# Kernel optimization log

Hardware: AMD Instinct MI355X
Metric: run time of the kernel (lower is better)

Reference implementation:

```python
import jax, jax.numpy as jnp
import numpy as np

ND, NW, E, D, DOUT = 20000, 30000, 500000, 256, 256


def setup_inputs() -> dict:
    key = jax.random.key(0)
    ks = jax.random.split(key, 10)
    inp = {
        "doc_hidden": jax.random.normal(ks[0], (ND, D), dtype=jnp.float32),
        "word_hidden": jax.random.normal(ks[1], (NW, D), dtype=jnp.float32),
        "edge_doc": jax.random.randint(ks[2], (E,), 0, ND),
        "edge_word": jax.random.randint(ks[3], (E,), 0, NW),
        # attn_fc_d2w / attn_fc_w2d: Linear(2*D, 1)
        "attn_d2w_w": jax.random.normal(ks[4], (2 * D, 1), dtype=jnp.float32) / np.sqrt(2 * D),
        "attn_d2w_b": jnp.zeros((1,), dtype=jnp.float32),
        "attn_w2d_w": jax.random.normal(ks[5], (2 * D, 1), dtype=jnp.float32) / np.sqrt(2 * D),
        "attn_w2d_b": jnp.zeros((1,), dtype=jnp.float32),
        # fc: Linear(D, DOUT), shared by doc and word outputs
        "fc_w": jax.random.normal(ks[6], (D, DOUT), dtype=jnp.float32) / np.sqrt(D),
        "fc_b": jnp.zeros((DOUT,), dtype=jnp.float32),
    }
    return inp


def _segment_softmax(e, seg, n):
    # e: [E] edge scores, seg: [E] destination ids -> per-dst softmax
    m = jax.ops.segment_max(e, seg, num_segments=n)
    ex = jnp.exp(e - m[seg])
    s = jax.ops.segment_sum(ex, seg, num_segments=n)
    return ex / jnp.maximum(s[seg], 1e-30)


def _gat_direction(z_src_nodes, z_dst_nodes, src_idx, dst_idx, w, b, n_dst):
    D_ = z_src_nodes.shape[1]
    zs = z_src_nodes[src_idx]                      # [E, D]
    zd = z_dst_nodes[dst_idx]                      # [E, D]
    # concat([zs, zd]) @ w == zs @ w[:D] + zd @ w[D:]
    a = zs @ w[:D_] + zd @ w[D_:] + b              # [E, 1]
    e = jax.nn.leaky_relu(a[:, 0], negative_slope=0.01)  # [E]
    alpha = _segment_softmax(e, dst_idx, n_dst)    # [E]
    return jax.ops.segment_sum(alpha[:, None] * zs, dst_idx, num_segments=n_dst)


def reference(doc_hidden, word_hidden, edge_doc, edge_word,
              attn_d2w_w, attn_d2w_b, attn_w2d_w, attn_w2d_b, fc_w, fc_b):
    # 'include': doc -> word aggregation into word nodes
    word_h = _gat_direction(doc_hidden, word_hidden, edge_doc, edge_word,
                            attn_d2w_w, attn_d2w_b, NW)
    # 'included': word -> doc aggregation into doc nodes
    doc_h = _gat_direction(word_hidden, doc_hidden, edge_word, edge_doc,
                           attn_w2d_w, attn_w2d_b, ND)
    # shared fc; dropout is identity in eval; softmax over feature dim (dim=1)
    doc_out = jax.nn.softmax(doc_h @ fc_w + fc_b, axis=1)
    word_out = jax.nn.softmax(word_h @ fc_w + fc_b, axis=1)
    return doc_out, word_out
```

## Files before the change

### kernel.cpp

```cpp
#include <hip/hip_runtime.h>

constexpr int ND_N = 20000;
constexpr int NW_N = 30000;
constexpr int NE_E = 500000;
constexpr int DDIM = 256;
constexpr int MROWS = ND_N + NW_N;

constexpr int SB = 64;

constexpr float QSCALE = 32767.f / 8.f;
constexpr float DQSCALE = 8.f / 32767.f;

constexpr int LROW = DDIM + 8;

constexpr int EDGE_BLOCKS = (NE_E + 255) / 256;
constexpr int NODE_BLOCKS = (MROWS + 3) / 4;
constexpr int CONV_BLOCKS = DDIM;

typedef __attribute__((ext_vector_type(8))) short short8v;
typedef __attribute__((ext_vector_type(4))) float f32x4;
typedef __attribute__((ext_vector_type(4))) short s16x4;
typedef __attribute__((ext_vector_type(4))) unsigned short us4;

__device__ __forceinline__ float lrelu(float x) { return x > 0.f ? x : 0.01f * x; }
__device__ __forceinline__ unsigned short f2bf(float x) {
  unsigned u = __float_as_uint(x);
  return (unsigned short)((u + 0x7FFFu + ((u >> 16) & 1u)) >> 16);
}
__device__ __forceinline__ float bf2f(unsigned short h) {
  return __uint_as_float(((unsigned)h) << 16);
}
__device__ __forceinline__ short q16(float x) {
  float c = fminf(fmaxf(x, -8.f), 8.f);
  return (short)__float2int_rn(c * QSCALE);
}

__global__ __launch_bounds__(256) void prep_all(
    const float* __restrict__ doc, const float* __restrict__ word,
    const float* __restrict__ d2w_w, const float* __restrict__ w2d_w,
    const float* __restrict__ fc_w,
    const int* __restrict__ ed, const int* __restrict__ ew,
    float* __restrict__ s1, float* __restrict__ t2,
    float* __restrict__ s2, float* __restrict__ t1,
    short* __restrict__ doc_q, short* __restrict__ word_q,
    int* __restrict__ pos1, int* __restrict__ pos2,
    unsigned short* __restrict__ bkt1, unsigned short* __restrict__ bkt2,
    unsigned short* __restrict__ whi, unsigned short* __restrict__ wlo) {
  int b = blockIdx.x;
  if (b < EDGE_BLOCKS) {
    int i = b * 256 + threadIdx.x;
    if (i >= NE_E) return;
    int d = ed[i], w = ew[i];
    int p1 = atomicAdd(&pos1[w], 1);
    p1 = min(p1, SB - 1);
    __builtin_nontemporal_store((unsigned short)d, &bkt1[(size_t)w * SB + p1]);
    int p2 = atomicAdd(&pos2[d], 1);
    p2 = min(p2, SB - 1);
    __builtin_nontemporal_store((unsigned short)w, &bkt2[(size_t)d * SB + p2]);
  } else if (b < EDGE_BLOCKS + NODE_BLOCKS) {
    int wid = (b - EDGE_BLOCKS) * 4 + (threadIdx.x >> 6);
    int lane = threadIdx.x & 63;
    if (wid >= MROWS) return;
    const float* h;
    const float* wa;
    const float* wb;
    float* oa;
    float* ob;
    short* qdst;
    int idx;
    if (wid < ND_N) {
      idx = wid;
      h = doc + (size_t)idx * DDIM;
      wa = d2w_w;
      wb = w2d_w + DDIM;
      oa = s1;
      ob = t2;
      qdst = doc_q;
    } else {
      idx = wid - ND_N;
      h = word + (size_t)idx * DDIM;
      wa = w2d_w;
      wb = d2w_w + DDIM;
      oa = s2;
      ob = t1;
      qdst = word_q;
    }
    const float4 z = *(const float4*)&h[lane * 4];
    const float4 a4 = *(const float4*)&wa[lane * 4];
    const float4 b4 = *(const float4*)&wb[lane * 4];
    s16x4 zq;
    zq.x = q16(z.x);
    zq.y = q16(z.y);
    zq.z = q16(z.z);
    zq.w = q16(z.w);
    *(s16x4*)&qdst[(size_t)idx * DDIM + lane * 4] = zq;
    float pa = z.x * a4.x + z.y * a4.y + z.z * a4.z + z.w * a4.w;
    float pb = z.x * b4.x + z.y * b4.y + z.z * b4.z + z.w * b4.w;
#pragma unroll
    for (int o = 32; o > 0; o >>= 1) {
      pa += __shfl_xor(pa, o);
      pb += __shfl_xor(pb, o);
    }
    if (lane == 0) {
      oa[idx] = pa;
      ob[idx] = pb;
    }
  } else {
    int k = b - EDGE_BLOCKS - NODE_BLOCKS;
    int n = threadIdx.x;
    float x = fc_w[(size_t)k * DDIM + n];
    unsigned short h = f2bf(x);
    float lo = x - bf2f(h);
    whi[(size_t)n * DDIM + k] = h;
    wlo[(size_t)n * DDIM + k] = f2bf(lo);
  }
}

__global__ __launch_bounds__(256) void aggregate_all(
    const short* __restrict__ doc_q, const short* __restrict__ word_q,
    const unsigned short* __restrict__ bkt1, const unsigned short* __restrict__ bkt2,
    const int* __restrict__ pos1, const int* __restrict__ pos2,
    const float* __restrict__ s1, const float* __restrict__ t1,
    const float* __restrict__ s2, const float* __restrict__ t2,
    const float* __restrict__ b1p, const float* __restrict__ b2p,
    float* __restrict__ out) {
  int wid = (blockIdx.x * blockDim.x + threadIdx.x) >> 6;
  int lane = threadIdx.x & 63;
  if (wid >= MROWS) return;
  const short* src;
  const unsigned short* bkt;
  const float* sS;
  float tval, bval;
  int cnt, row;
  if (wid < NW_N) {
    src = doc_q;
    bkt = bkt1 + (size_t)wid * SB;
    cnt = min(pos1[wid], SB);
    sS = s1;
    tval = t1[wid];
    bval = b1p[0];
    row = ND_N + wid;
  } else {
    int d = wid - NW_N;
    src = word_q;
    bkt = bkt2 + (size_t)d * SB;
    cnt = min(pos2[d], SB);
    sS = s2;
    tval = t2[d];
    bval = b2p[0];
    row = d;
  }
  int sidx = 0;
  float v = 0.f;
  if (lane < cnt) {
    sidx = bkt[lane];
    v = __expf(lrelu(sS[sidx] + tval + bval));
  }
  float vsum = v;
  float ax = 0.f, ay = 0.f, az = 0.f, aw = 0.f;
  int t = 0;
  for (; t + 16 <= cnt; t += 16) {
    s16x4 z16[16];
    float vv[16];
#pragma unroll
    for (int q = 0; q < 16; ++q) {
      int ss = __shfl(sidx, t + q);
      vv[q] = __shfl(v, t + q);
      z16[q] = *(const s16x4*)&src[(size_t)ss * DDIM + lane * 4];
    }
#pragma unroll
    for (int q = 0; q < 16; ++q) {
      ax += vv[q] * (float)z16[q].x;
      ay += vv[q] * (float)z16[q].y;
      az += vv[q] * (float)z16[q].z;
      aw += vv[q] * (float)z16[q].w;
    }
  }
  for (; t + 8 <= cnt; t += 8) {
    s16x4 z8[8];
    float vv[8];
#pragma unroll
    for (int q = 0; q < 8; ++q) {
      int ss = __shfl(sidx, t + q);
      vv[q] = __shfl(v, t + q);
      z8[q] = *(const s16x4*)&src[(size_t)ss * DDIM + lane * 4];
    }
#pragma unroll
    for (int q = 0; q < 8; ++q) {
      ax += vv[q] * (float)z8[q].x;
      ay += vv[q] * (float)z8[q].y;
      az += vv[q] * (float)z8[q].z;
      aw += vv[q] * (float)z8[q].w;
    }
  }
  for (; t < cnt; ++t) {
    int ss = __shfl(sidx, t);
    float vv = __shfl(v, t);
    const s16x4 z = *(const s16x4*)&src[(size_t)ss * DDIM + lane * 4];
    ax += vv * (float)z.x;
    ay += vv * (float)z.y;
    az += vv * (float)z.z;
    aw += vv * (float)z.w;
  }
#pragma unroll
  for (int o = 32; o > 0; o >>= 1) vsum += __shfl_xor(vsum, o);
  float inv = DQSCALE / fmaxf(vsum, 1e-30f);
  float4 o4 = {ax * inv, ay * inv, az * inv, aw * inv};
  *(float4*)&out[(size_t)row * DDIM + lane * 4] = o4;
}

__global__ __launch_bounds__(256) void fc_mfma_sm(
    float* __restrict__ y,
    const unsigned short* __restrict__ w_hi_t, const unsigned short* __restrict__ w_lo_t,
    const float* __restrict__ bias, int nrows) {
  __shared__ unsigned short a_hi[32 * LROW];
  __shared__ unsigned short a_lo[32 * LROW];
  __shared__ float lds_max[4][32];
  __shared__ float lds_sum[4][32];
  int tid = threadIdx.x;
  int row0 = blockIdx.x * 32;

  int wv = tid >> 6;
  int l = tid & 63;
  int lr = l & 15;
  int g = l >> 4;
  int lk = g * 8;

  const unsigned short* bh = w_hi_t + (size_t)(wv * 64 + lr) * DDIM + lk;
  const unsigned short* bl = w_lo_t + (size_t)(wv * 64 + lr) * DDIM + lk;
  short8v bHi[2][4], bLo[2][4];
#pragma unroll
  for (int cf = 0; cf < 4; ++cf) {
    bHi[0][cf] = *(const short8v*)(bh + cf * 16 * DDIM);
    bLo[0][cf] = *(const short8v*)(bl + cf * 16 * DDIM);
  }

  {
    int r = tid >> 3;
    int c0 = (tid & 7) * 32;
    int arow = min(row0 + r, nrows - 1);
    const float* srcp = &y[(size_t)arow * DDIM + c0];
    unsigned short* dh = &a_hi[r * LROW + c0];
    unsigned short* dl = &a_lo[r * LROW + c0];
#pragma unroll
    for (int j = 0; j < 8; ++j) {
      float4 f = *(const float4*)&srcp[j * 4];
      float fv[4] = {f.x, f.y, f.z, f.w};
      us4 h4, l4;
#pragma unroll
      for (int c = 0; c < 4; ++c) {
        unsigned short hb = f2bf(fv[c]);
        h4[c] = hb;
        l4[c] = f2bf(fv[c] - bf2f(hb));
      }
      *(us4*)&dh[j * 4] = h4;
      *(us4*)&dl[j * 4] = l4;
    }
  }
  __syncthreads();

  f32x4 acc[2][4];
#pragma unroll
  for (int rf = 0; rf < 2; ++rf)
#pragma unroll
    for (int cf = 0; cf < 4; ++cf) acc[rf][cf] = (f32x4){0.f, 0.f, 0.f, 0.f};

#pragma unroll
  for (int ks = 0; ks < 8; ++ks) {
    const int cur = ks & 1;
    const int nxt = cur ^ 1;
    if (ks < 7) {
#pragma unroll
      for (int cf = 0; cf < 4; ++cf) {
        bHi[nxt][cf] = *(const short8v*)(bh + cf * 16 * DDIM + (ks + 1) * 32);
        bLo[nxt][cf] = *(const short8v*)(bl + cf * 16 * DDIM + (ks + 1) * 32);
      }
    }
    int kbase = ks * 32 + lk;
    short8v aHi[2], aLo[2];
#pragma unroll
    for (int rf = 0; rf < 2; ++rf) {
      int r = rf * 16 + lr;
      aHi[rf] = *(const short8v*)&a_hi[r * LROW + kbase];
      aLo[rf] = *(const short8v*)&a_lo[r * LROW + kbase];
    }
#pragma unroll
    for (int rf = 0; rf < 2; ++rf)
#pragma unroll
      for (int cf = 0; cf < 4; ++cf) {
        acc[rf][cf] = __builtin_amdgcn_mfma_f32_16x16x32_bf16(aHi[rf], bHi[cur][cf], acc[rf][cf], 0, 0, 0);
        acc[rf][cf] = __builtin_amdgcn_mfma_f32_16x16x32_bf16(aLo[rf], bHi[cur][cf], acc[rf][cf], 0, 0, 0);
        acc[rf][cf] = __builtin_amdgcn_mfma_f32_16x16x32_bf16(aHi[rf], bLo[cur][cf], acc[rf][cf], 0, 0, 0);
      }
  }

#pragma unroll
  for (int rf = 0; rf < 2; ++rf)
#pragma unroll
    for (int cf = 0; cf < 4; ++cf) {
      float bc = bias[wv * 64 + cf * 16 + lr];
#pragma unroll
      for (int r = 0; r < 4; ++r) acc[rf][cf][r] += bc;
    }

#pragma unroll
  for (int rf = 0; rf < 2; ++rf)
#pragma unroll
    for (int r = 0; r < 4; ++r) {
      float m = fmaxf(fmaxf(acc[rf][0][r], acc[rf][1][r]), fmaxf(acc[rf][2][r], acc[rf][3][r]));
#pragma unroll
      for (int o = 1; o < 16; o <<= 1) m = fmaxf(m, __shfl_xor(m, o));
      if (lr == 0) lds_max[wv][rf * 16 + g * 4 + r] = m;
    }
  __syncthreads();
#pragma unroll
  for (int rf = 0; rf < 2; ++rf)
#pragma unroll
    for (int r = 0; r < 4; ++r) {
      int idx = rf * 16 + g * 4 + r;
      float m = fmaxf(fmaxf(lds_max[0][idx], lds_max[1][idx]),
                      fmaxf(lds_max[2][idx], lds_max[3][idx]));
      float s = 0.f;
#pragma unroll
      for (int cf = 0; cf < 4; ++cf) {
        float e = __expf(acc[rf][cf][r] - m);
        acc[rf][cf][r] = e;
        s += e;
      }
#pragma unroll
      for (int o = 1; o < 16; o <<= 1) s += __shfl_xor(s, o);
      if (lr == 0) lds_sum[wv][idx] = s;
    }
  __syncthreads();
#pragma unroll
  for (int rf = 0; rf < 2; ++rf)
#pragma unroll
    for (int r = 0; r < 4; ++r) {
      int idx = rf * 16 + g * 4 + r;
      float s = lds_sum[0][idx] + lds_sum[1][idx] + lds_sum[2][idx] + lds_sum[3][idx];
      float inv = 1.f / s;
      int row = row0 + rf * 16 + g * 4 + r;
      if (row < nrows) {
#pragma unroll
        for (int cf = 0; cf < 4; ++cf)
          y[(size_t)row * DDIM + wv * 64 + cf * 16 + lr] = acc[rf][cf][r] * inv;
      }
    }
}

extern "C" void kernel_launch(void* const* d_in, const int* in_sizes, int n_in,
                              void* d_out, int out_size, void* d_ws, size_t ws_size,
                              hipStream_t stream) {
  const float* doc_hidden = (const float*)d_in[0];
  const float* word_hidden = (const float*)d_in[1];
  const int* edge_doc = (const int*)d_in[2];
  const int* edge_word = (const int*)d_in[3];
  const float* d2w_w = (const float*)d_in[4];
  const float* d2w_b = (const float*)d_in[5];
  const float* w2d_w = (const float*)d_in[6];
  const float* w2d_b = (const float*)d_in[7];
  const float* fc_w = (const float*)d_in[8];
  const float* fc_b = (const float*)d_in[9];
  float* out = (float*)d_out;

  char* p = (char*)d_ws;
  auto carveB = [&](size_t bytes) {
    char* r = p;
    p += ((bytes + 255) & ~(size_t)255);
    return r;
  };
  auto carve = [&](size_t elems) { return carveB(elems * 4); };
  float* s1 = (float*)carve(ND_N);
  float* t2 = (float*)carve(ND_N);
  float* s2 = (float*)carve(NW_N);
  float* t1 = (float*)carve(NW_N);
  char* zbeg = p;
  int* pos1 = (int*)carve(NW_N);
  int* pos2 = (int*)carve(ND_N);
  char* zend = p;
  unsigned short* bkt1 = (unsigned short*)carveB((size_t)NW_N * SB * 2);
  unsigned short* bkt2 = (unsigned short*)carveB((size_t)ND_N * SB * 2);
  short* doc_q = (short*)carveB((size_t)ND_N * DDIM * 2);
  short* word_q = (short*)carveB((size_t)NW_N * DDIM * 2);
  unsigned short* w_hi_t = (unsigned short*)carveB((size_t)DDIM * DDIM * 2);
  unsigned short* w_lo_t = (unsigned short*)carveB((size_t)DDIM * DDIM * 2);

  hipMemsetAsync(zbeg, 0, (size_t)(zend - zbeg), stream);

  prep_all<<<EDGE_BLOCKS + NODE_BLOCKS + CONV_BLOCKS, 256, 0, stream>>>(
      doc_hidden, word_hidden, d2w_w, w2d_w, fc_w, edge_doc, edge_word,
      s1, t2, s2, t1, doc_q, word_q, pos1, pos2, bkt1, bkt2, w_hi_t, w_lo_t);

  aggregate_all<<<(MROWS + 3) / 4, 256, 0, stream>>>(doc_q, word_q, bkt1, bkt2, pos1, pos2,
                                                     s1, t1, s2, t2, d2w_b, w2d_b, out);

  fc_mfma_sm<<<(MROWS + 31) / 32, 256, 0, stream>>>(out, w_hi_t, w_lo_t, fc_b, MROWS);
}
```

Measured before the change: 313.9 us.

## Make FC kernel persistent with prefetched double-buffered tiles; pad atomic counters

The FC+softmax kernel now runs as a persistent grid of 521 blocks, each handling 3 row tiles. The next tile's fp32 rows are prefetched into registers during the current tile's MFMA work, then split to bf16 hi/lo into a second LDS buffer. This hides global load latency and cuts block launch overhead. Separately, the per-node edge counters are spaced 16 ints apart (one per 64-byte line) so atomics from different nodes no longer share a cache line. The cost is a 16x larger counter memset and scattered counter reads.

```diff
diff --git a/kernel.cpp b/kernel.cpp
--- a/kernel.cpp
+++ b/kernel.cpp
@@ -7,6 +7,7 @@
 constexpr int MROWS = ND_N + NW_N;
 
 constexpr int SB = 64;
+constexpr int PSTR = 16;
 
 constexpr float QSCALE = 32767.f / 8.f;
 constexpr float DQSCALE = 8.f / 32767.f;
@@ -16,6 +17,10 @@
 constexpr int EDGE_BLOCKS = (NE_E + 255) / 256;
 constexpr int NODE_BLOCKS = (MROWS + 3) / 4;
 constexpr int CONV_BLOCKS = DDIM;
+
+constexpr int FC_TILES = (MROWS + 31) / 32;
+constexpr int FC_BLOCKS = 521;
+constexpr int FC_ITERS = 3;
 
 typedef __attribute__((ext_vector_type(8))) short short8v;
 typedef __attribute__((ext_vector_type(4))) float f32x4;
@@ -51,10 +56,10 @@
     int i = b * 256 + threadIdx.x;
     if (i >= NE_E) return;
     int d = ed[i], w = ew[i];
-    int p1 = atomicAdd(&pos1[w], 1);
+    int p1 = atomicAdd(&pos1[(size_t)w * PSTR], 1);
     p1 = min(p1, SB - 1);
     __builtin_nontemporal_store((unsigned short)d, &bkt1[(size_t)w * SB + p1]);
-    int p2 = atomicAdd(&pos2[d], 1);
+    int p2 = atomicAdd(&pos2[(size_t)d * PSTR], 1);
     p2 = min(p2, SB - 1);
     __builtin_nontemporal_store((unsigned short)w, &bkt2[(size_t)d * SB + p2]);
   } else if (b < EDGE_BLOCKS + NODE_BLOCKS) {
@@ -135,7 +140,7 @@
   if (wid < NW_N) {
     src = doc_q;
     bkt = bkt1 + (size_t)wid * SB;
-    cnt = min(pos1[wid], SB);
+    cnt = min(pos1[(size_t)wid * PSTR], SB);
     sS = s1;
     tval = t1[wid];
     bval = b1p[0];
@@ -144,7 +149,7 @@
     int d = wid - NW_N;
     src = word_q;
     bkt = bkt2 + (size_t)d * SB;
-    cnt = min(pos2[d], SB);
+    cnt = min(pos2[(size_t)d * PSTR], SB);
     sS = s2;
     tval = t2[d];
     bval = b2p[0];
@@ -213,39 +218,41 @@
     float* __restrict__ y,
     const unsigned short* __restrict__ w_hi_t, const unsigned short* __restrict__ w_lo_t,
     const float* __restrict__ bias, int nrows) {
-  __shared__ unsigned short a_hi[32 * LROW];
-  __shared__ unsigned short a_lo[32 * LROW];
+  __shared__ unsigned short a_hi[2][32 * LROW];
+  __shared__ unsigned short a_lo[2][32 * LROW];
   __shared__ float lds_max[4][32];
   __shared__ float lds_sum[4][32];
   int tid = threadIdx.x;
-  int row0 = blockIdx.x * 32;
-
   int wv = tid >> 6;
   int l = tid & 63;
   int lr = l & 15;
   int g = l >> 4;
   int lk = g * 8;
+  int sr = tid >> 3;
+  int sc0 = (tid & 7) * 32;
 
   const unsigned short* bh = w_hi_t + (size_t)(wv * 64 + lr) * DDIM + lk;
   const unsigned short* bl = w_lo_t + (size_t)(wv * 64 + lr) * DDIM + lk;
+
+  float4 sreg[8];
+  {
+    int arow = min(blockIdx.x * 32 + sr, nrows - 1);
+    const float* sp = &y[(size_t)arow * DDIM + sc0];
+#pragma unroll
+    for (int j = 0; j < 8; ++j) sreg[j] = *(const float4*)&sp[j * 4];
+  }
   short8v bHi[2][4], bLo[2][4];
 #pragma unroll
   for (int cf = 0; cf < 4; ++cf) {
     bHi[0][cf] = *(const short8v*)(bh + cf * 16 * DDIM);
     bLo[0][cf] = *(const short8v*)(bl + cf * 16 * DDIM);
   }
-
   {
-    int r = tid >> 3;
-    int c0 = (tid & 7) * 32;
-    int arow = min(row0 + r, nrows - 1);
-    const float* srcp = &y[(size_t)arow * DDIM + c0];
-    unsigned short* dh = &a_hi[r * LROW + c0];
-    unsigned short* dl = &a_lo[r * LROW + c0];
+    unsigned short* dh = &a_hi[0][sr * LROW + sc0];
+    unsigned short* dl = &a_lo[0][sr * LROW + sc0];
 #pragma unroll
     for (int j = 0; j < 8; ++j) {
-      float4 f = *(const float4*)&srcp[j * 4];
-      float fv[4] = {f.x, f.y, f.z, f.w};
+      float fv[4] = {sreg[j].x, sreg[j].y, sreg[j].z, sreg[j].w};
       us4 h4, l4;
 #pragma unroll
       for (int c = 0; c < 4; ++c) {
@@ -259,93 +266,132 @@
   }
   __syncthreads();
 
-  f32x4 acc[2][4];
-#pragma unroll
-  for (int rf = 0; rf < 2; ++rf)
-#pragma unroll
-    for (int cf = 0; cf < 4; ++cf) acc[rf][cf] = (f32x4){0.f, 0.f, 0.f, 0.f};
-
-#pragma unroll
-  for (int ks = 0; ks < 8; ++ks) {
-    const int cur = ks & 1;
-    const int nxt = cur ^ 1;
-    if (ks < 7) {
+  int cur = 0;
+  for (int it = 0; it < FC_ITERS; ++it) {
+    int row0 = (blockIdx.x + it * FC_BLOCKS) * 32;
+
+    if (it + 1 < FC_ITERS) {
+      int arow = min((blockIdx.x + (it + 1) * FC_BLOCKS) * 32 + sr, nrows - 1);
+      const float* sp = &y[(size_t)arow * DDIM + sc0];
+#pragma unroll
+      for (int j = 0; j < 8; ++j) sreg[j] = *(const float4*)&sp[j * 4];
+    }
+
+    f32x4 acc[2][4];
+#pragma unroll
+    for (int rf = 0; rf < 2; ++rf)
+#pragma unroll
+      for (int cf = 0; cf < 4; ++cf) acc[rf][cf] = (f32x4){0.f, 0.f, 0.f, 0.f};
+
+#pragma unroll
+    for (int ks = 0; ks < 8; ++ks) {
+      const int cb = ks & 1;
+      const int nb = cb ^ 1;
+      if (ks < 7) {
+#pragma unroll
+        for (int cf = 0; cf < 4; ++cf) {
+          bHi[nb][cf] = *(const short8v*)(bh + cf * 16 * DDIM + (ks + 1) * 32);
+          bLo[nb][cf] = *(const short8v*)(bl + cf * 16 * DDIM + (ks + 1) * 32);
+        }
+      }
+      int kbase = ks * 32 + lk;
+      short8v aHi[2], aLo[2];
+#pragma unroll
+      for (int rf = 0; rf < 2; ++rf) {
+        int r = rf * 16 + lr;
+        aHi[rf] = *(const short8v*)&a_hi[cur][r * LROW + kbase];
+        aLo[rf] = *(const short8v*)&a_lo[cur][r * LROW + kbase];
+      }
+#pragma unroll
+      for (int rf = 0; rf < 2; ++rf)
+#pragma unroll
+        for (int cf = 0; cf < 4; ++cf) {
+          acc[rf][cf] = __builtin_amdgcn_mfma_f32_16x16x32_bf16(aHi[rf], bHi[cb][cf], acc[rf][cf], 0, 0, 0);
+          acc[rf][cf] = __builtin_amdgcn_mfma_f32_16x16x32_bf16(aLo[rf], bHi[cb][cf], acc[rf][cf], 0, 0, 0);
+          acc[rf][cf] = __builtin_amdgcn_mfma_f32_16x16x32_bf16(aHi[rf], bLo[cb][cf], acc[rf][cf], 0, 0, 0);
+        }
+    }
+    if (it + 1 < FC_ITERS) {
 #pragma unroll
       for (int cf = 0; cf < 4; ++cf) {
-        bHi[nxt][cf] = *(const short8v*)(bh + cf * 16 * DDIM + (ks + 1) * 32);
-        bLo[nxt][cf] = *(const short8v*)(bl + cf * 16 * DDIM + (ks + 1) * 32);
-      }
-    }
-    int kbase = ks * 32 + lk;
-    short8v aHi[2], aLo[2];
-#pragma unroll
-    for (int rf = 0; rf < 2; ++rf) {
-      int r = rf * 16 + lr;
-      aHi[rf] = *(const short8v*)&a_hi[r * LROW + kbase];
-      aLo[rf] = *(const short8v*)&a_lo[r * LROW + kbase];
-    }
+        bHi[0][cf] = *(const short8v*)(bh + cf * 16 * DDIM);
+        bLo[0][cf] = *(const short8v*)(bl + cf * 16 * DDIM);
+      }
+    }
+
 #pragma unroll
     for (int rf = 0; rf < 2; ++rf)
 #pragma unroll
       for (int cf = 0; cf < 4; ++cf) {
-        acc[rf][cf] = __builtin_amdgcn_mfma_f32_16x16x32_bf16(aHi[rf], bHi[cur][cf], acc[rf][cf], 0, 0, 0);
-        acc[rf][cf] = __builtin_amdgcn_mfma_f32_16x16x32_bf16(aLo[rf], bHi[cur][cf], acc[rf][cf], 0, 0, 0);
-        acc[rf][cf] = __builtin_amdgcn_mfma_f32_16x16x32_bf16(aHi[rf], bLo[cur][cf], acc[rf][cf], 0, 0, 0);
-      }
-  }
-
-#pragma unroll
-  for (int rf = 0; rf < 2; ++rf)
-#pragma unroll
-    for (int cf = 0; cf < 4; ++cf) {
-      float bc = bias[wv * 64 + cf * 16 + lr];
-#pragma unroll
-      for (int r = 0; r < 4; ++r) acc[rf][cf][r] += bc;
-    }
-
-#pragma unroll
-  for (int rf = 0; rf < 2; ++rf)
-#pragma unroll
-    for (int r = 0; r < 4; ++r) {
-      float m = fmaxf(fmaxf(acc[rf][0][r], acc[rf][1][r]), fmaxf(acc[rf][2][r], acc[rf][3][r]));
-#pragma unroll
-      for (int o = 1; o < 16; o <<= 1) m = fmaxf(m, __shfl_xor(m, o));
-      if (lr == 0) lds_max[wv][rf * 16 + g * 4 + r] = m;
-    }
-  __syncthreads();
-#pragma unroll
-  for (int rf = 0; rf < 2; ++rf)
-#pragma unroll
-    for (int r = 0; r < 4; ++r) {
-      int idx = rf * 16 + g * 4 + r;
-      float m = fmaxf(fmaxf(lds_max[0][idx], lds_max[1][idx]),
-                      fmaxf(lds_max[2][idx], lds_max[3][idx]));
-      float s = 0.f;
-#pragma unroll
-      for (int cf = 0; cf < 4; ++cf) {
-        float e = __expf(acc[rf][cf][r] - m);
-        acc[rf][cf][r] = e;
-        s += e;
-      }
-#pragma unroll
-      for (int o = 1; o < 16; o <<= 1) s += __shfl_xor(s, o);
-      if (lr == 0) lds_sum[wv][idx] = s;
-    }
-  __syncthreads();
-#pragma unroll
-  for (int rf = 0; rf < 2; ++rf)
-#pragma unroll
-    for (int r = 0; r < 4; ++r) {
-      int idx = rf * 16 + g * 4 + r;
-      float s = lds_sum[0][idx] + lds_sum[1][idx] + lds_sum[2][idx] + lds_sum[3][idx];
-      float inv = 1.f / s;
-      int row = row0 + rf * 16 + g * 4 + r;
-      if (row < nrows) {
-#pragma unroll
-        for (int cf = 0; cf < 4; ++cf)
-          y[(size_t)row * DDIM + wv * 64 + cf * 16 + lr] = acc[rf][cf][r] * inv;
-      }
-    }
+        float bc = bias[wv * 64 + cf * 16 + lr];
+#pragma unroll
+        for (int r = 0; r < 4; ++r) acc[rf][cf][r] += bc;
+      }
+#pragma unroll
+    for (int rf = 0; rf < 2; ++rf)
+#pragma unroll
+      for (int r = 0; r < 4; ++r) {
+        float m = fmaxf(fmaxf(acc[rf][0][r], acc[rf][1][r]), fmaxf(acc[rf][2][r], acc[rf][3][r]));
+#pragma unroll
+        for (int o = 1; o < 16; o <<= 1) m = fmaxf(m, __shfl_xor(m, o));
+        if (lr == 0) lds_max[wv][rf * 16 + g * 4 + r] = m;
+      }
+    __syncthreads();
+#pragma unroll
+    for (int rf = 0; rf < 2; ++rf)
+#pragma unroll
+      for (int r = 0; r < 4; ++r) {
+        int idx = rf * 16 + g * 4 + r;
+        float m = fmaxf(fmaxf(lds_max[0][idx], lds_max[1][idx]),
+                        fmaxf(lds_max[2][idx], lds_max[3][idx]));
+        float s = 0.f;
+#pragma unroll
+        for (int cf = 0; cf < 4; ++cf) {
+          float e = __expf(acc[rf][cf][r] - m);
+          acc[rf][cf][r] = e;
+          s += e;
+        }
+#pragma unroll
+        for (int o = 1; o < 16; o <<= 1) s += __shfl_xor(s, o);
+        if (lr == 0) lds_sum[wv][idx] = s;
+      }
+    __syncthreads();
+#pragma unroll
+    for (int rf = 0; rf < 2; ++rf)
+#pragma unroll
+      for (int r = 0; r < 4; ++r) {
+        int idx = rf * 16 + g * 4 + r;
+        float s = lds_sum[0][idx] + lds_sum[1][idx] + lds_sum[2][idx] + lds_sum[3][idx];
+        float inv = 1.f / s;
+        int row = row0 + rf * 16 + g * 4 + r;
+        if (row < nrows) {
+#pragma unroll
+          for (int cf = 0; cf < 4; ++cf)
+            y[(size_t)row * DDIM + wv * 64 + cf * 16 + lr] = acc[rf][cf][r] * inv;
+        }
+      }
+
+    if (it + 1 < FC_ITERS) {
+      int nxt = cur ^ 1;
+      unsigned short* dh = &a_hi[nxt][sr * LROW + sc0];
+      unsigned short* dl = &a_lo[nxt][sr * LROW + sc0];
+#pragma unroll
+      for (int j = 0; j < 8; ++j) {
+        float fv[4] = {sreg[j].x, sreg[j].y, sreg[j].z, sreg[j].w};
+        us4 h4, l4;
+#pragma unroll
+        for (int c = 0; c < 4; ++c) {
+          unsigned short hb = f2bf(fv[c]);
+          h4[c] = hb;
+          l4[c] = f2bf(fv[c] - bf2f(hb));
+        }
+        *(us4*)&dh[j * 4] = h4;
+        *(us4*)&dl[j * 4] = l4;
+      }
+      __syncthreads();
+      cur = nxt;
+    }
+  }
 }
 
 extern "C" void kernel_launch(void* const* d_in, const int* in_sizes, int n_in,
@@ -375,8 +421,8 @@
   float* s2 = (float*)carve(NW_N);
   float* t1 = (float*)carve(NW_N);
   char* zbeg = p;
-  int* pos1 = (int*)carve(NW_N);
-  int* pos2 = (int*)carve(ND_N);
+  int* pos1 = (int*)carve((size_t)NW_N * PSTR);
+  int* pos2 = (int*)carve((size_t)ND_N * PSTR);
   char* zend = p;
   unsigned short* bkt1 = (unsigned short*)carveB((size_t)NW_N * SB * 2);
   unsigned short* bkt2 = (unsigned short*)carveB((size_t)ND_N * SB * 2);
@@ -394,5 +440,5 @@
   aggregate_all<<<(MROWS + 3) / 4, 256, 0, stream>>>(doc_q, word_q, bkt1, bkt2, pos1, pos2,
                                                      s1, t1, s2, t2, d2w_b, w2d_b, out);
 
-  fc_mfma_sm<<<(MROWS + 31) / 32, 256, 0, stream>>>(out, w_hi_t, w_lo_t, fc_b, MROWS);
-}
+  fc_mfma_sm<<<FC_BLOCKS, 256, 0, stream>>>(out, w_hi_t, w_lo_t, fc_b, MROWS);
+}
```

Measured after the change: 351.3 us. 11.9% more time.
